# Optimization experiments

Hardware: AMD Instinct MI355X
Metric: run time of the kernel (lower is better)

## Reference

```python
import jax, jax.numpy as jnp
import numpy as np

B, S, D, H = 2, 2048, 1024, 16
HD = D // H  # head_dim = 64


def setup_inputs() -> dict:
    key = jax.random.key(0)
    k1, k2, k3 = jax.random.split(key, 3)
    return {
        "hidden_states": jax.random.normal(k1, (B, S, D), dtype=jnp.float32),
        "W_attn": jax.random.normal(k2, (D, 3 * D), dtype=jnp.float32) * 0.02,
        "b_attn": jnp.zeros((3 * D,), dtype=jnp.float32),
        "W_proj": jax.random.normal(k3, (D, D), dtype=jnp.float32) * 0.02,
        "b_proj": jnp.zeros((D,), dtype=jnp.float32),
    }


def reference(hidden_states, W_attn, b_attn, W_proj, b_proj):
    b, s, d = hidden_states.shape
    qkv = hidden_states @ W_attn + b_attn  # [b, s, 3d]
    q, k, v = jnp.split(qkv, 3, axis=-1)

    def split_heads(x):  # [b, s, d] -> [b, H, s, hd]
        return x.reshape(b, s, H, HD).transpose(0, 2, 1, 3)

    q, k, v = split_heads(q), split_heads(k), split_heads(v)

    # scores: [b, H, s, s]
    w = jnp.einsum("bhqd,bhkd->bhqk", q, k) / jnp.sqrt(jnp.float32(HD))
    causal = jnp.tril(jnp.ones((s, s), dtype=bool))  # [s, s]
    mask_value = jnp.finfo(w.dtype).min
    w = jnp.where(causal[None, None, :, :], w, mask_value)
    w = jax.nn.softmax(w, axis=-1)

    score = jnp.einsum("bhqk,bhkd->bhqd", w, v)  # [b, H, s, hd]
    score = score.transpose(0, 2, 1, 3).reshape(b, s, d)
    out = score @ W_proj + b_proj
    return out
```

## Files before the change

kernel.cpp:

```cpp
#include <hip/hip_runtime.h>
#include <hip/hip_bf16.h>

typedef unsigned short bf16_t;
typedef __attribute__((ext_vector_type(8))) short bf16x8;
typedef __attribute__((ext_vector_type(4))) short bf16x4;
typedef __attribute__((ext_vector_type(4))) float f32x4;

#define MFMA16(a, b, c) __builtin_amdgcn_mfma_f32_16x16x32_bf16((a), (b), (c), 0, 0, 0)

__device__ __forceinline__ bf16_t f2bf(float f) {
  union { float f; unsigned u; } v; v.f = f;
  unsigned u = v.u;
  u += 0x7FFFu + ((u >> 16) & 1u);
  return (bf16_t)(u >> 16);
}

__device__ __forceinline__ unsigned cvt_pk_bf16(float lo, float hi) {
  unsigned r;
  asm volatile("v_cvt_pk_bf16_f32 %0, %1, %2" : "=v"(r) : "v"(lo), "v"(hi));
  return r;
}

__device__ __forceinline__ unsigned pack2(short lo, short hi) {
  return ((unsigned)(unsigned short)lo) | ((unsigned)(unsigned short)hi << 16);
}

__device__ __forceinline__ void gld_lds16(const void* g, void* l) {
  __builtin_amdgcn_global_load_lds(
      (const __attribute__((address_space(1))) unsigned int*)g,
      (__attribute__((address_space(3))) unsigned int*)l, 16, 0, 0);
}

__global__ __launch_bounds__(256) void k_prep(const float* __restrict__ X,
                                              bf16_t* __restrict__ Xb,
                                              const float* __restrict__ Wa,
                                              bf16_t* __restrict__ WaT,
                                              const float* __restrict__ Wp,
                                              bf16_t* __restrict__ WpT) {
  __shared__ bf16_t t[64][65];
  const int blk = blockIdx.x;
  const int tid = threadIdx.x;
  if (blk < 2048) {
    int i = blk * 256 + tid;
    const float4* p = (const float4*)X + (size_t)i * 2;
    float4 a = p[0], b = p[1];
    bf16x8 o;
    o[0] = (short)f2bf(a.x); o[1] = (short)f2bf(a.y); o[2] = (short)f2bf(a.z); o[3] = (short)f2bf(a.w);
    o[4] = (short)f2bf(b.x); o[5] = (short)f2bf(b.y); o[6] = (short)f2bf(b.z); o[7] = (short)f2bf(b.w);
    *((bf16x8*)Xb + i) = o;
    return;
  }
  const bool wa = (blk < 2816);
  const int bx = wa ? (blk - 2048) : (blk - 2816);
  const int NX = wa ? 48 : 16;
  const int N = wa ? 3072 : 1024;
  const int K = 1024;
  const float* W = wa ? Wa : Wp;
  bf16_t* Wt = wa ? WaT : WpT;
  const int n0 = (bx % NX) * 64, k0 = (bx / NX) * 64;
#pragma unroll
  for (int p = 0; p < 16; ++p) {
    int lin = p * 256 + tid;
    int r = lin >> 6, c = lin & 63;
    t[r][c] = f2bf(W[(size_t)(k0 + r) * N + n0 + c]);
  }
  __syncthreads();
#pragma unroll
  for (int p = 0; p < 16; ++p) {
    int lin = p * 256 + tid;
    int nr = lin >> 6, kc = lin & 63;
    Wt[(size_t)(n0 + nr) * K + k0 + kc] = t[kc][nr];
  }
}

template <bool BF16OUT, bool SCALEQ, int BM, int BN, int TPB>
__global__ __launch_bounds__(TPB) void k_gemm_bt(const bf16_t* __restrict__ A,
                                                 const bf16_t* __restrict__ Bt,
                                                 const float* __restrict__ bias,
                                                 void* __restrict__ Cout, int M, int N, int K,
                                                 int nx) {
  constexpr int WN = (TPB == 512) ? 4 : 2;
  constexpr int WM = (TPB / 64) / WN;
  constexpr int WTM = BM / WM;
  constexpr int WTN = BN / WN;
  constexpr int NI = WTM / 16;
  constexpr int NJ = WTN / 16;
  constexpr int PA = BM * 4 / TPB;
  constexpr int PB = BN * 4 / TPB;
  __shared__ bf16_t Al[2][BM * 32];
  __shared__ bf16_t Bl[2][BN * 32];
  const int tid = threadIdx.x;
  const int lane = tid & 63;
  const int wid = tid >> 6;
  const int wm = wid / WN, wn = wid % WN;
  const int nwg = gridDim.x;
  const int cpx = nwg >> 3;
  const int swz = (blockIdx.x & 7) * cpx + (blockIdx.x >> 3);
  const int m0 = (swz / nx) * BM, n0 = (swz % nx) * BN;
  const int lr = lane & 15;
  const int lk = lane >> 4;

  f32x4 acc[NI][NJ] = {};

  auto STAGE = [&](int buf, int k0) {
#pragma unroll
    for (int p = 0; p < PA; ++p) {
      int o = p * TPB * 16 + tid * 16;
      int row = o >> 6, cb = o & 63;
      gld_lds16((const char*)A + ((size_t)(m0 + row) * K + k0) * 2 + cb,
                (char*)Al[buf] + o);
    }
#pragma unroll
    for (int p = 0; p < PB; ++p) {
      int o = p * TPB * 16 + tid * 16;
      int row = o >> 6, cb = o & 63;
      gld_lds16((const char*)Bt + ((size_t)(n0 + row) * K + k0) * 2 + cb,
                (char*)Bl[buf] + o);
    }
  };

  STAGE(0, 0);

  const int nk = K >> 5;
  for (int t = 0; t < nk; ++t) {
    const int cur = t & 1;
    asm volatile("s_waitcnt vmcnt(0)" ::: "memory");
    __builtin_amdgcn_s_barrier();
    if (t + 1 < nk) STAGE(cur ^ 1, (t + 1) << 5);
    bf16x8 af[NI], bfr[NJ];
#pragma unroll
    for (int i = 0; i < NI; ++i)
      af[i] = *(const bf16x8*)(Al[cur] + ((wm * WTM + i * 16 + lr) * 32 + lk * 8));
#pragma unroll
    for (int j = 0; j < NJ; ++j)
      bfr[j] = *(const bf16x8*)(Bl[cur] + ((wn * WTN + j * 16 + lr) * 32 + lk * 8));
#pragma unroll
    for (int i = 0; i < NI; ++i)
#pragma unroll
      for (int j = 0; j < NJ; ++j)
        acc[i][j] = MFMA16(af[i], bfr[j], acc[i][j]);
  }

#pragma unroll
  for (int i = 0; i < NI; ++i) {
    int grow = m0 + wm * WTM + i * 16 + lk * 4;
#pragma unroll
    for (int j = 0; j < NJ; ++j) {
      int gcol = n0 + wn * WTN + j * 16 + lr;
      float bv = bias[gcol];
      float scl = (SCALEQ && gcol < 1024) ? 0.18033688011112042f : 1.0f;
#pragma unroll
      for (int r = 0; r < 4; ++r) {
        float v = (acc[i][j][r] + bv) * scl;
        size_t off = (size_t)(grow + r) * N + gcol;
        if (BF16OUT)
          ((bf16_t*)Cout)[off] = f2bf(v);
        else
          ((float*)Cout)[off] = v;
      }
    }
  }
}

__global__ __launch_bounds__(256) void k_attn(const bf16_t* __restrict__ qkv,
                                              bf16_t* __restrict__ score) {
  __shared__ bf16_t Kl[2][64 * 64];
  __shared__ bf16_t Vt[2][64 * 64];
  __shared__ bf16_t Pl[4][16 * 64];
  const int tid = threadIdx.x;
  const int lane = tid & 63;
  const int w = tid >> 6;
  const int lr = lane & 15, lk = lane >> 4;

  const int flat = blockIdx.x;
  const int g = flat >> 5;
  const int idx = g & 7;
  const int grp = g >> 3;
  const int qt = (grp == 0) ? (31 - idx)
               : (grp == 1) ? (15 - idx)
               : (grp == 2) ? (16 + idx)
                            : idx;
  const int bh = flat & 31;
  const int b = bh >> 4, h = bh & 15;

  const bf16_t* Qb = qkv + (size_t)b * 2048 * 3072 + h * 64;
  const bf16_t* Kb = Qb + 1024;
  const bf16_t* Vb = Qb + 2048;

  int d0c[2], kv2[2], krow[2], kchk[2];
#pragma unroll
  for (int p = 0; p < 2; ++p) {
    int e = p * 256 + tid;
    d0c[p] = (e & 15) * 4;
    kv2[p] = (e >> 4) * 2;
    krow[p] = e >> 3;
    kchk[p] = (e & 7) ^ (krow[p] & 7);
  }

  const int qr0 = qt * 64 + w * 16;
  const int q = qr0 + lr;
  const int jtEnd = qt + 1;

  bf16x8 qf[2];
#pragma unroll
  for (int ks = 0; ks < 2; ++ks)
    qf[ks] = *(const bf16x8*)(Qb + (size_t)(qr0 + lr) * 3072 + ks * 32 + lk * 8);

  f32x4 o[4] = {};
  float l = 0.f;

  {
    bf16x4 v0[2][2];
#pragma unroll
    for (int p = 0; p < 2; ++p) {
      v0[p][0] = *(const bf16x4*)(Vb + (size_t)kv2[p] * 3072 + d0c[p]);
      v0[p][1] = *(const bf16x4*)(Vb + (size_t)(kv2[p] + 1) * 3072 + d0c[p]);
    }
#pragma unroll
    for (int p = 0; p < 2; ++p)
#pragma unroll
      for (int j = 0; j < 4; ++j) {
        int d = d0c[p] + j;
        int addr = (d * 128 + kv2[p] * 2) ^ (((d & 7) ^ ((d >> 3) & 7)) << 4);
        *(unsigned*)((char*)Vt + addr) = pack2(v0[p][0][j], v0[p][1][j]);
      }
  }
  bf16x4 vrA[2][2], vrB[2][2];
#pragma unroll
  for (int p = 0; p < 2; ++p) {
    vrA[p][0] = *(const bf16x4*)(Vb + (size_t)(64 + kv2[p]) * 3072 + d0c[p]);
    vrA[p][1] = *(const bf16x4*)(Vb + (size_t)(64 + kv2[p] + 1) * 3072 + d0c[p]);
  }
#pragma unroll
  for (int p = 0; p < 2; ++p)
    gld_lds16((const char*)Kb + ((size_t)krow[p] * 3072 + kchk[p] * 8) * 2,
              (char*)Kl + (p * 256 + tid) * 16);

  auto STEP = [&](int jt, bf16x4 (&vrC)[2][2], bf16x4 (&vrN)[2][2], bool last) {
    const int kv0 = jt * 64;
    asm volatile("s_waitcnt lgkmcnt(0)" ::: "memory");
    __builtin_amdgcn_s_barrier();
    char* wbase = (char*)Vt + (((jt + 1) & 1) << 13);
#pragma unroll
    for (int p = 0; p < 2; ++p)
#pragma unroll
      for (int j = 0; j < 4; ++j) {
        int d = d0c[p] + j;
        int addr = (d * 128 + kv2[p] * 2) ^ (((d & 7) ^ ((d >> 3) & 7)) << 4);
        *(unsigned*)(wbase + addr) = pack2(vrC[p][0][j], vrC[p][1][j]);
      }
    if (!last) {
      const int kvV = (kv0 + 128 < 2048) ? kv0 + 128 : 1920;
#pragma unroll
      for (int p = 0; p < 2; ++p) {
        vrN[p][0] = *(const bf16x4*)(Vb + (size_t)(kvV + kv2[p]) * 3072 + d0c[p]);
        vrN[p][1] = *(const bf16x4*)(Vb + (size_t)(kvV + kv2[p] + 1) * 3072 + d0c[p]);
      }
      char* kbase = (char*)Kl + (((jt + 1) & 1) << 13);
#pragma unroll
      for (int p = 0; p < 2; ++p)
        gld_lds16((const char*)Kb + ((size_t)(kv0 + 64 + krow[p]) * 3072 + kchk[p] * 8) * 2,
                  kbase + (p * 256 + tid) * 16);
      asm volatile("s_waitcnt vmcnt(6)" ::: "memory");
    } else {
      asm volatile("s_waitcnt vmcnt(0)" ::: "memory");
    }
    const char* kread = (const char*)Kl + ((jt & 1) << 13);
    bf16x8 kf[4][2];
#pragma unroll
    for (int nc = 0; nc < 4; ++nc) {
      const char* rowp = kread + (nc * 16 + lr) * 128;
      kf[nc][0] = *(const bf16x8*)(rowp + ((lk ^ (lr & 7)) << 4));
      kf[nc][1] = *(const bf16x8*)(rowp + (((4 | lk) ^ (lr & 7)) << 4));
    }
    f32x4 s[4];
    __builtin_amdgcn_s_setprio(1);
#pragma unroll
    for (int nc = 0; nc < 4; ++nc) {
      f32x4 z = {};
      z = MFMA16(kf[nc][0], qf[0], z);
      z = MFMA16(kf[nc][1], qf[1], z);
      s[nc] = z;
    }
    __builtin_amdgcn_s_setprio(0);
    if (kv0 + 63 > qr0) {
#pragma unroll
      for (int nc = 0; nc < 4; ++nc)
#pragma unroll
        for (int r = 0; r < 4; ++r) {
          int kvi = kv0 + nc * 16 + lk * 4 + r;
          if (kvi > q) s[nc][r] = -INFINITY;
        }
    }
#pragma unroll
    for (int nc = 0; nc < 4; ++nc)
#pragma unroll
      for (int r = 0; r < 4; ++r) {
        float p = exp2f(s[nc][r]);
        s[nc][r] = p;
        l += p;
      }
    bf16_t* Pw = Pl[w];
#pragma unroll
    for (int nc = 0; nc < 4; ++nc) {
      uint2 u;
      u.x = cvt_pk_bf16(s[nc][0], s[nc][1]);
      u.y = cvt_pk_bf16(s[nc][2], s[nc][3]);
      int addr = (lr * 128 + (nc * 16 + lk * 4) * 2) ^ ((lr & 7) << 4);
      *(uint2*)((char*)Pw + addr) = u;
    }
    const char* rbase = (const char*)Vt + ((jt & 1) << 13);
    bf16x8 pa[2];
#pragma unroll
    for (int ks = 0; ks < 2; ++ks) {
      int addr = (lr * 128 + ks * 64 + lk * 16) ^ ((lr & 7) << 4);
      pa[ks] = *(const bf16x8*)((const char*)Pl[w] + addr);
    }
    __builtin_amdgcn_s_setprio(1);
#pragma unroll
    for (int db = 0; db < 4; ++db)
#pragma unroll
      for (int ks = 0; ks < 2; ++ks) {
        int d = db * 16 + lr;
        int addr = (d * 128 + ks * 64 + lk * 16) ^ (((d & 7) ^ ((d >> 3) & 7)) << 4);
        bf16x8 vb = *(const bf16x8*)(rbase + addr);
        o[db] = MFMA16(vb, pa[ks], o[db]);
      }
    __builtin_amdgcn_s_setprio(0);
  };

  int jt = 0;
  for (;;) {
    STEP(jt, vrA, vrB, jt + 1 == jtEnd);
    if (++jt == jtEnd) break;
    STEP(jt, vrB, vrA, jt + 1 == jtEnd);
    if (++jt == jtEnd) break;
  }

  l += __shfl_xor(l, 16);
  l += __shfl_xor(l, 32);
  const float rl = 1.0f / l;
  bf16_t* orow = score + (size_t)(b * 2048 + q) * 1024 + h * 64 + lk * 4;
#pragma unroll
  for (int db = 0; db < 4; ++db) {
    unsigned w0 = cvt_pk_bf16(o[db][0] * rl, o[db][1] * rl);
    unsigned w1 = cvt_pk_bf16(o[db][2] * rl, o[db][3] * rl);
    uint2 pkt; pkt.x = w0; pkt.y = w1;
    *(uint2*)(orow + db * 16) = pkt;
  }
}

extern "C" void kernel_launch(void* const* d_in, const int* in_sizes, int n_in,
                              void* d_out, int out_size, void* d_ws, size_t ws_size,
                              hipStream_t stream) {
  const float* X  = (const float*)d_in[0];
  const float* Wa = (const float*)d_in[1];
  const float* ba = (const float*)d_in[2];
  const float* Wp = (const float*)d_in[3];
  const float* bp = (const float*)d_in[4];
  float* out = (float*)d_out;

  char* ws = (char*)d_ws;
  bf16_t* Xb  = (bf16_t*)ws;
  bf16_t* WaT = (bf16_t*)(ws + (size_t)(8u << 20));
  bf16_t* WpT = (bf16_t*)(ws + (size_t)(14u << 20));
  bf16_t* QKV = (bf16_t*)(ws + (size_t)(16u << 20));
  bf16_t* S_  = Xb;

  k_prep<<<3072, 256, 0, stream>>>(X, Xb, Wa, WaT, Wp, WpT);
  k_gemm_bt<true, true, 128, 128, 512><<<768, 512, 0, stream>>>(Xb, WaT, ba, QKV, 4096, 3072, 1024, 24);
  k_attn<<<1024, 256, 0, stream>>>(QKV, S_);
  k_gemm_bt<false, false, 64, 64, 256><<<1024, 256, 0, stream>>>(S_, WpT, bp, out, 4096, 1024, 1024, 16);
}
```

Before: 108.4 us.

## Add dedicated QKV GEMM with K=64 tiles, XOR-swizzled LDS, and XCD block swizzle

Replaces the generic templated GEMM for the QKV projection with a specialized kernel that loads 64-wide K tiles directly into LDS using an XOR chunk swizzle to avoid bank conflicts. It remaps block indices across the 8 XCDs so neighbouring tiles share L2. The kernel is single-buffered with two barriers per iteration, which may lose the overlap the old double-buffered version had. The generic GEMM drops the Q-scaling template parameter.

```diff
diff --git a/kernel.cpp b/kernel.cpp
--- a/kernel.cpp
+++ b/kernel.cpp
@@ -73,7 +73,84 @@
   }
 }
 
-template <bool BF16OUT, bool SCALEQ, int BM, int BN, int TPB>
+template <bool SCALEQ>
+__global__ __launch_bounds__(512) void k_gemm_qkv(const bf16_t* __restrict__ A,
+                                                  const bf16_t* __restrict__ Bt,
+                                                  const float* __restrict__ bias,
+                                                  bf16_t* __restrict__ Cout,
+                                                  int M, int N, int K, int nx) {
+  __shared__ bf16_t Al[128 * 64];
+  __shared__ bf16_t Bl[128 * 64];
+  const int tid = threadIdx.x;
+  const int lane = tid & 63;
+  const int wid = tid >> 6;
+  const int wm = wid >> 2, wn = wid & 3;
+  const int nwg = gridDim.x;
+  const int cpx = nwg >> 3;
+  const int swz = (blockIdx.x & 7) * cpx + (blockIdx.x >> 3);
+  const int m0 = (swz / nx) * 128, n0 = (swz % nx) * 128;
+  const int lr = lane & 15;
+  const int lk = lane >> 4;
+
+  int srow[2], schk[2];
+#pragma unroll
+  for (int p = 0; p < 2; ++p) {
+    int t2 = p * 512 + tid;
+    srow[p] = t2 >> 3;
+    schk[p] = (t2 & 7) ^ (srow[p] & 7);
+  }
+
+  f32x4 acc[4][2] = {};
+
+  for (int k0 = 0; k0 < K; k0 += 64) {
+    __syncthreads();
+#pragma unroll
+    for (int p = 0; p < 2; ++p) {
+      gld_lds16((const char*)A + ((size_t)(m0 + srow[p]) * K + k0 + schk[p] * 8) * 2,
+                (char*)Al + (p * 512 + tid) * 16);
+      gld_lds16((const char*)Bt + ((size_t)(n0 + srow[p]) * K + k0 + schk[p] * 8) * 2,
+                (char*)Bl + (p * 512 + tid) * 16);
+    }
+    __syncthreads();
+#pragma unroll
+    for (int kk = 0; kk < 2; ++kk) {
+      bf16x8 af[4], bfr[2];
+#pragma unroll
+      for (int i = 0; i < 4; ++i) {
+        int row = wm * 64 + i * 16 + lr;
+        af[i] = *(const bf16x8*)((const char*)Al + row * 128 + (((kk * 4 + lk) ^ (row & 7)) << 4));
+      }
+#pragma unroll
+      for (int j = 0; j < 2; ++j) {
+        int row = wn * 32 + j * 16 + lr;
+        bfr[j] = *(const bf16x8*)((const char*)Bl + row * 128 + (((kk * 4 + lk) ^ (row & 7)) << 4));
+      }
+#pragma unroll
+      for (int i = 0; i < 4; ++i)
+#pragma unroll
+        for (int j = 0; j < 2; ++j)
+          acc[i][j] = MFMA16(af[i], bfr[j], acc[i][j]);
+    }
+  }
+
+#pragma unroll
+  for (int i = 0; i < 4; ++i) {
+    int grow = m0 + wm * 64 + i * 16 + lk * 4;
+#pragma unroll
+    for (int j = 0; j < 2; ++j) {
+      int gcol = n0 + wn * 32 + j * 16 + lr;
+      float bv = bias[gcol];
+      float scl = (SCALEQ && gcol < 1024) ? 0.18033688011112042f : 1.0f;
+#pragma unroll
+      for (int r = 0; r < 4; ++r) {
+        float v = (acc[i][j][r] + bv) * scl;
+        Cout[(size_t)(grow + r) * N + gcol] = f2bf(v);
+      }
+    }
+  }
+}
+
+template <bool BF16OUT, int BM, int BN, int TPB>
 __global__ __launch_bounds__(TPB) void k_gemm_bt(const bf16_t* __restrict__ A,
                                                  const bf16_t* __restrict__ Bt,
                                                  const float* __restrict__ bias,
@@ -148,10 +225,9 @@
     for (int j = 0; j < NJ; ++j) {
       int gcol = n0 + wn * WTN + j * 16 + lr;
       float bv = bias[gcol];
-      float scl = (SCALEQ && gcol < 1024) ? 0.18033688011112042f : 1.0f;
 #pragma unroll
       for (int r = 0; r < 4; ++r) {
-        float v = (acc[i][j][r] + bv) * scl;
+        float v = acc[i][j][r] + bv;
         size_t off = (size_t)(grow + r) * N + gcol;
         if (BF16OUT)
           ((bf16_t*)Cout)[off] = f2bf(v);
@@ -368,7 +444,7 @@
   bf16_t* S_  = Xb;
 
   k_prep<<<3072, 256, 0, stream>>>(X, Xb, Wa, WaT, Wp, WpT);
-  k_gemm_bt<true, true, 128, 128, 512><<<768, 512, 0, stream>>>(Xb, WaT, ba, QKV, 4096, 3072, 1024, 24);
+  k_gemm_qkv<true><<<768, 512, 0, stream>>>(Xb, WaT, ba, QKV, 4096, 3072, 1024, 24);
   k_attn<<<1024, 256, 0, stream>>>(QKV, S_);
-  k_gemm_bt<false, false, 64, 64, 256><<<1024, 256, 0, stream>>>(S_, WpT, bp, out, 4096, 1024, 1024, 16);
-}
+  k_gemm_bt<false, 64, 64, 256><<<1024, 256, 0, stream>>>(S_, WpT, bp, out, 4096, 1024, 1024, 16);
+}
```

After: 103.7 us. 1.04x faster.

## Use BK=64 single-buffered GEMM with XOR-swizzled LDS layout

Applied to the files above, without the earlier changes.

The GEMM kernel now stages 64-wide K tiles instead of 32-wide ones and applies an XOR swizzle on 16-byte chunks in LDS to avoid bank conflicts on fragment reads. Double buffering is dropped in favour of a single buffer with two barriers per iteration. This halves the number of K-loop iterations and barriers, but it loses the overlap between global loads and MFMA compute.

```diff
diff --git a/kernel.cpp b/kernel.cpp
--- a/kernel.cpp
+++ b/kernel.cpp
@@ -74,21 +74,21 @@
 }
 
 template <bool BF16OUT, bool SCALEQ, int BM, int BN, int TPB>
-__global__ __launch_bounds__(TPB) void k_gemm_bt(const bf16_t* __restrict__ A,
-                                                 const bf16_t* __restrict__ Bt,
-                                                 const float* __restrict__ bias,
-                                                 void* __restrict__ Cout, int M, int N, int K,
-                                                 int nx) {
+__global__ __launch_bounds__(TPB) void k_gemm64(const bf16_t* __restrict__ A,
+                                                const bf16_t* __restrict__ Bt,
+                                                const float* __restrict__ bias,
+                                                void* __restrict__ Cout,
+                                                int M, int N, int K, int nx) {
   constexpr int WN = (TPB == 512) ? 4 : 2;
   constexpr int WM = (TPB / 64) / WN;
   constexpr int WTM = BM / WM;
   constexpr int WTN = BN / WN;
   constexpr int NI = WTM / 16;
   constexpr int NJ = WTN / 16;
-  constexpr int PA = BM * 4 / TPB;
-  constexpr int PB = BN * 4 / TPB;
-  __shared__ bf16_t Al[2][BM * 32];
-  __shared__ bf16_t Bl[2][BN * 32];
+  constexpr int PA = BM * 8 / TPB;
+  constexpr int PB = BN * 8 / TPB;
+  __shared__ bf16_t Al[BM * 64];
+  __shared__ bf16_t Bl[BN * 64];
   const int tid = threadIdx.x;
   const int lane = tid & 63;
   const int wid = tid >> 6;
@@ -100,45 +100,52 @@
   const int lr = lane & 15;
   const int lk = lane >> 4;
 
+  int srowA[PA], schkA[PA], srowB[PB], schkB[PB];
+#pragma unroll
+  for (int p = 0; p < PA; ++p) {
+    int t2 = p * TPB + tid;
+    srowA[p] = t2 >> 3;
+    schkA[p] = (t2 & 7) ^ (srowA[p] & 7);
+  }
+#pragma unroll
+  for (int p = 0; p < PB; ++p) {
+    int t2 = p * TPB + tid;
+    srowB[p] = t2 >> 3;
+    schkB[p] = (t2 & 7) ^ (srowB[p] & 7);
+  }
+
   f32x4 acc[NI][NJ] = {};
 
-  auto STAGE = [&](int buf, int k0) {
-#pragma unroll
-    for (int p = 0; p < PA; ++p) {
-      int o = p * TPB * 16 + tid * 16;
-      int row = o >> 6, cb = o & 63;
-      gld_lds16((const char*)A + ((size_t)(m0 + row) * K + k0) * 2 + cb,
-                (char*)Al[buf] + o);
-    }
-#pragma unroll
-    for (int p = 0; p < PB; ++p) {
-      int o = p * TPB * 16 + tid * 16;
-      int row = o >> 6, cb = o & 63;
-      gld_lds16((const char*)Bt + ((size_t)(n0 + row) * K + k0) * 2 + cb,
-                (char*)Bl[buf] + o);
-    }
-  };
-
-  STAGE(0, 0);
-
-  const int nk = K >> 5;
-  for (int t = 0; t < nk; ++t) {
-    const int cur = t & 1;
-    asm volatile("s_waitcnt vmcnt(0)" ::: "memory");
-    __builtin_amdgcn_s_barrier();
-    if (t + 1 < nk) STAGE(cur ^ 1, (t + 1) << 5);
-    bf16x8 af[NI], bfr[NJ];
-#pragma unroll
-    for (int i = 0; i < NI; ++i)
-      af[i] = *(const bf16x8*)(Al[cur] + ((wm * WTM + i * 16 + lr) * 32 + lk * 8));
-#pragma unroll
-    for (int j = 0; j < NJ; ++j)
-      bfr[j] = *(const bf16x8*)(Bl[cur] + ((wn * WTN + j * 16 + lr) * 32 + lk * 8));
-#pragma unroll
-    for (int i = 0; i < NI; ++i)
-#pragma unroll
-      for (int j = 0; j < NJ; ++j)
-        acc[i][j] = MFMA16(af[i], bfr[j], acc[i][j]);
+  for (int k0 = 0; k0 < K; k0 += 64) {
+    __syncthreads();
+#pragma unroll
+    for (int p = 0; p < PA; ++p)
+      gld_lds16((const char*)A + ((size_t)(m0 + srowA[p]) * K + k0 + schkA[p] * 8) * 2,
+                (char*)Al + (p * TPB + tid) * 16);
+#pragma unroll
+    for (int p = 0; p < PB; ++p)
+      gld_lds16((const char*)Bt + ((size_t)(n0 + srowB[p]) * K + k0 + schkB[p] * 8) * 2,
+                (char*)Bl + (p * TPB + tid) * 16);
+    __syncthreads();
+#pragma unroll
+    for (int kk = 0; kk < 2; ++kk) {
+      bf16x8 af[NI], bfr[NJ];
+#pragma unroll
+      for (int i = 0; i < NI; ++i) {
+        int row = wm * WTM + i * 16 + lr;
+        af[i] = *(const bf16x8*)((const char*)Al + row * 128 + (((kk * 4 + lk) ^ (row & 7)) << 4));
+      }
+#pragma unroll
+      for (int j = 0; j < NJ; ++j) {
+        int row = wn * WTN + j * 16 + lr;
+        bfr[j] = *(const bf16x8*)((const char*)Bl + row * 128 + (((kk * 4 + lk) ^ (row & 7)) << 4));
+      }
+#pragma unroll
+      for (int i = 0; i < NI; ++i)
+#pragma unroll
+        for (int j = 0; j < NJ; ++j)
+          acc[i][j] = MFMA16(af[i], bfr[j], acc[i][j]);
+    }
   }
 
 #pragma unroll
@@ -368,7 +375,7 @@
   bf16_t* S_  = Xb;
 
   k_prep<<<3072, 256, 0, stream>>>(X, Xb, Wa, WaT, Wp, WpT);
-  k_gemm_bt<true, true, 128, 128, 512><<<768, 512, 0, stream>>>(Xb, WaT, ba, QKV, 4096, 3072, 1024, 24);
+  k_gemm64<true, true, 128, 128, 512><<<768, 512, 0, stream>>>(Xb, WaT, ba, QKV, 4096, 3072, 1024, 24);
   k_attn<<<1024, 256, 0, stream>>>(QKV, S_);
-  k_gemm_bt<false, false, 64, 64, 256><<<1024, 256, 0, stream>>>(S_, WpT, bp, out, 4096, 1024, 1024, 16);
-}
+  k_gemm64<false, false, 64, 64, 256><<<1024, 256, 0, stream>>>(S_, WpT, bp, out, 4096, 1024, 1024, 16);
+}
```

After: 102.6 us, median of 2. -5.3%, faster.
